# Optimization experiments

Measured on AMD Instinct MI355X. Metric: run time of the kernel, lower is better.

The kernel has to match this reference:

```python
import jax, jax.numpy as jnp
import numpy as np

N, E, D, H, G, OUT = 50000, 800000, 128, 128, 64, 10


def setup_inputs() -> dict:
    key = jax.random.key(0)
    ks = jax.random.split(key, 10)
    x = jax.random.normal(ks[0], (N, D), dtype=jnp.float32)
    edge_index = jax.random.randint(ks[1], (2, E), 0, N, dtype=jnp.int64)
    batch = jnp.sort(jax.random.randint(ks[2], (N,), 0, G, dtype=jnp.int64))
    s = 1.0 / np.sqrt(D)
    W0 = jax.random.normal(ks[3], (D, H), dtype=jnp.float32) * s
    W1 = jax.random.normal(ks[4], (H, H), dtype=jnp.float32) * s
    W2 = jax.random.normal(ks[5], (H, H), dtype=jnp.float32) * s
    M0w = jax.random.normal(ks[6], (H, H), dtype=jnp.float32) * s
    M0b = jnp.zeros((H,), dtype=jnp.float32)
    M1w = jax.random.normal(ks[7], (H, OUT), dtype=jnp.float32) * s
    M1b = jnp.zeros((OUT,), dtype=jnp.float32)
    return dict(x=x, W0=W0, W1=W1, W2=W2, M0w=M0w, M0b=M0b, M1w=M1w, M1b=M1b,
                edge_index=edge_index, batch=batch)


def gcn_conv(x, W, src, dst):
    # PyG GCNConv (bias=False): h = x @ W; out = D^-1/2 (A + I) D^-1/2 h
    h = x @ W
    deg = jnp.zeros((N,), h.dtype).at[dst].add(1.0) + 1.0  # +1 for self-loop
    dinv = deg ** -0.5
    w = dinv[src] * dinv[dst]  # [E]
    agg = jax.ops.segment_sum(h[src] * w[:, None], dst, num_segments=N)
    return agg + h * (dinv * dinv)[:, None]  # self-loop term


def reference(x, W0, W1, W2, M0w, M0b, M1w, M1b, edge_index, batch):
    src, dst = edge_index[0], edge_index[1]
    h = gcn_conv(x, W0, src, dst)
    h = gcn_conv(jax.nn.relu(h), W1, src, dst)
    h = gcn_conv(jax.nn.relu(h), W2, src, dst)
    # global mean pool over graphs
    sums = jax.ops.segment_sum(h, batch, num_segments=G)
    cnts = jax.ops.segment_sum(jnp.ones((N,), h.dtype), batch, num_segments=G)
    pooled = sums / jnp.maximum(cnts, 1.0)[:, None]
    out = pooled @ M0w + M0b
    out = jax.nn.relu(out) @ M1w + M1b
    return out
```

## Files before the change

kernel.cpp:

```cpp
#include <hip/hip_runtime.h>
#include <hip/hip_fp16.h>

#define NN 50000
#define NE 800000
#define DIM 128
#define NG 64
#define NOUT 10

#define NBKT 391
#define HBLK 256
#define CHUNK ((NE + HBLK - 1) / HBLK)
#define PSLICE 8

#define WPAD 136
#define PSTR (DIM * WPAD)

typedef __attribute__((ext_vector_type(8))) short short8;
typedef __attribute__((ext_vector_type(8))) _Float16 half8;
typedef __attribute__((ext_vector_type(2))) __fp16 fp16x2;
typedef __attribute__((ext_vector_type(4))) float float4v;

union S8H8 { short8 s; half8 h; };
union SH { short s; _Float16 h; };
union H8P { short8 s; fp16x2 h2[4]; };

__device__ __forceinline__ void f16_split(float v, short& hi, short& lo) {
    SH a, b;
    a.h = (_Float16)v;
    b.h = (_Float16)(v - (float)a.h);
    hi = a.s;
    lo = b.s;
}

#define PREP_WB 48
#define PREP_HB (PREP_WB + HBLK)
#define PREP_NB (PREP_HB + 1)
__global__ __launch_bounds__(256) void prep_kernel(const float* __restrict__ W0,
                                                   const float* __restrict__ W1,
                                                   const float* __restrict__ W2,
                                                   short* __restrict__ wsp,
                                                   const int* __restrict__ ei,
                                                   int* __restrict__ blkhist,
                                                   const int* __restrict__ batch,
                                                   int* __restrict__ first) {
    __shared__ int h[NBKT];
    int bx = blockIdx.x;
    if (bx < PREP_WB) {
        int w = bx >> 4;
        int sub = bx & 15;
        const float* W = (w == 0) ? W0 : (w == 1) ? W1 : W2;
        short* Wh = wsp + w * 2 * PSTR;
        short* Wl = Wh + PSTR;
        #pragma unroll
        for (int t = 0; t < 4; ++t) {
            int idx = sub * 1024 + t * 256 + threadIdx.x;
            int k = idx >> 7, n = idx & 127;
            int phys = n * WPAD + ((k + 8 * (n >> 3)) & 127);
            short hi, lo;
            f16_split(W[idx], hi, lo);
            Wh[phys] = hi;
            Wl[phys] = lo;
        }
    } else if (bx < PREP_HB) {
        int b = bx - PREP_WB;
        for (int i = threadIdx.x; i < NBKT; i += 256) h[i] = 0;
        __syncthreads();
        int lo = b * CHUNK, hi = min(lo + CHUNK, NE);
        for (int e = lo + threadIdx.x; e < hi; e += 256)
            atomicAdd(&h[ei[NE + e] >> 7], 1);
        __syncthreads();
        for (int i = threadIdx.x; i < NBKT; i += 256)
            blkhist[b * NBKT + i] = h[i];
    } else {
        int g = threadIdx.x;
        if (g <= NG) {
            int lo = 0, hi = NN;
            while (lo < hi) {
                int mid = (lo + hi) >> 1;
                if (batch[mid] < g) lo = mid + 1; else hi = mid;
            }
            first[g] = lo;
        }
    }
}

__global__ __launch_bounds__(256) void scan_all(int* __restrict__ blkhist,
                                                int* __restrict__ bintot) {
    __shared__ int s[256];
    int bin = blockIdx.x;
    int t = threadIdx.x;
    int v = blkhist[t * NBKT + bin];
    s[t] = v;
    __syncthreads();
    #pragma unroll
    for (int off = 1; off < 256; off <<= 1) {
        int tv = (t >= off) ? s[t - off] : 0;
        __syncthreads();
        s[t] += tv;
        __syncthreads();
    }
    blkhist[t * NBKT + bin] = s[t] - v;
    if (t == 255) bintot[bin] = s[255];
}

__global__ __launch_bounds__(512) void base_scan_kernel(const int* __restrict__ bintot,
                                                        int* __restrict__ bucket_base) {
    __shared__ int s[512];
    int t = threadIdx.x;
    int v = (t < NBKT) ? bintot[t] : 0;
    s[t] = v;
    __syncthreads();
    #pragma unroll
    for (int off = 1; off < 512; off <<= 1) {
        int tv = (t >= off) ? s[t - off] : 0;
        __syncthreads();
        s[t] += tv;
        __syncthreads();
    }
    if (t <= NBKT) bucket_base[t] = s[t] - v;
}

__global__ __launch_bounds__(256) void bucket_scatter(const int* __restrict__ ei,
                                                      const int* __restrict__ blkhist,
                                                      const int* __restrict__ bucket_base,
                                                      unsigned* __restrict__ ebuf) {
    __shared__ int cur[NBKT];
    int b = blockIdx.x;
    for (int i = threadIdx.x; i < NBKT; i += 256)
        cur[i] = blkhist[b * NBKT + i] + bucket_base[i];
    __syncthreads();
    int lo = b * CHUNK, hi = min(lo + CHUNK, NE);
    for (int e = lo + threadIdx.x; e < hi; e += 256) {
        int s = ei[e];
        int d = ei[NE + e];
        int pos = atomicAdd(&cur[d >> 7], 1);
        ebuf[pos] = ((unsigned)(d & 127) << 16) | (unsigned)s;
    }
}

__global__ __launch_bounds__(128) void build_csr(const unsigned* __restrict__ ebuf,
                                                 const int* __restrict__ bucket_base,
                                                 int* __restrict__ rowoff,
                                                 int* __restrict__ csr_src,
                                                 float* __restrict__ dinv) {
    __shared__ int deg[128];
    __shared__ int loff[128];
    int g = blockIdx.x;
    int lo = bucket_base[g], hi = bucket_base[g + 1];
    int t = threadIdx.x;
    deg[t] = 0;
    __syncthreads();
    for (int p = lo + t; p < hi; p += 128)
        atomicAdd(&deg[ebuf[p] >> 16], 1);
    __syncthreads();
    int v = deg[t];
    loff[t] = v;
    __syncthreads();
    #pragma unroll
    for (int off = 1; off < 128; off <<= 1) {
        int tv = (t >= off) ? loff[t - off] : 0;
        __syncthreads();
        loff[t] += tv;
        __syncthreads();
    }
    int excl = loff[t] - v;
    int node = g * 128 + t;
    if (node < NN) {
        rowoff[node] = lo + excl;
        dinv[node] = 1.0f / sqrtf((float)v + 1.0f);
    }
    if (node == 0) rowoff[NN] = NE;
    deg[t] = lo + excl;
    __syncthreads();
    for (int p = lo + t; p < hi; p += 128) {
        unsigned pk = ebuf[p];
        int pos = atomicAdd(&deg[pk >> 16], 1);
        csr_src[pos] = (int)(pk & 0xFFFFu);
    }
}

template <bool AF32>
__global__ __launch_bounds__(256) void gemm_mfma(const float* __restrict__ Xf,
                                                 const __half* __restrict__ Xh,
                                                 const short* __restrict__ Wsp,
                                                 __half* __restrict__ Y, int nrows) {
    __shared__ short W2p[2 * PSTR];
    int tid = threadIdx.x;
    {
        const short8* g = (const short8*)Wsp;
        #pragma unroll
        for (int i = 0; i < 17; ++i) {
            int e = tid + 256 * i;
            *(short8*)&W2p[e * 8] = g[e];
        }
    }
    int wave = tid >> 6;
    int lane = tid & 63;
    int lm = lane & 15;
    int lq = lane >> 4;
    int row_t0 = blockIdx.x * 128 + wave * 32;

    float4v acc[2][8];
    #pragma unroll
    for (int t = 0; t < 2; ++t)
        #pragma unroll
        for (int i = 0; i < 8; ++i) acc[t][i] = (float4v){0.f, 0.f, 0.f, 0.f};

    __syncthreads();
    #pragma unroll
    for (int kk = 0; kk < 4; ++kk) {
        half8 a[2];
        #pragma unroll
        for (int t = 0; t < 2; ++t) {
            int r = min(row_t0 + t * 16 + lm, nrows - 1);
            size_t ao = (size_t)r * DIM + kk * 32 + lq * 8;
            if (AF32) {
                float4 xa = *(const float4*)(Xf + ao);
                float4 xb = *(const float4*)(Xf + ao + 4);
                a[t][0] = (_Float16)xa.x; a[t][1] = (_Float16)xa.y;
                a[t][2] = (_Float16)xa.z; a[t][3] = (_Float16)xa.w;
                a[t][4] = (_Float16)xb.x; a[t][5] = (_Float16)xb.y;
                a[t][6] = (_Float16)xb.z; a[t][7] = (_Float16)xb.w;
            } else {
                S8H8 u;
                u.s = *(const short8*)((const short*)Xh + ao);
                a[t] = u.h;
            }
        }
        int pk = (kk * 32 + lq * 8 + 8 * lm) & 127;
        #pragma unroll
        for (int n0 = 0; n0 < 8; ++n0) {
            int base = (lm * 8 + n0) * WPAD + pk;
            S8H8 bh, bl;
            bh.s = *(const short8*)&W2p[base];
            bl.s = *(const short8*)&W2p[PSTR + base];
            #pragma unroll
            for (int t = 0; t < 2; ++t) {
                acc[t][n0] = __builtin_amdgcn_mfma_f32_16x16x32_f16(a[t], bh.h, acc[t][n0], 0, 0, 0);
                acc[t][n0] = __builtin_amdgcn_mfma_f32_16x16x32_f16(a[t], bl.h, acc[t][n0], 0, 0, 0);
            }
        }
    }
    #pragma unroll
    for (int t = 0; t < 2; ++t)
        #pragma unroll
        for (int rg = 0; rg < 4; ++rg) {
            int row = row_t0 + t * 16 + lq * 4 + rg;
            if (row < nrows) {
                H8P o;
                #pragma unroll
                for (int j = 0; j < 4; ++j)
                    o.h2[j] = __builtin_amdgcn_cvt_pkrtz(acc[t][2 * j][rg], acc[t][2 * j + 1][rg]);
                *(short8*)((short*)Y + (size_t)row * DIM + lm * 8) = o.s;
            }
        }
}

template <bool RELU>
__global__ __launch_bounds__(128) void agg_kernel(const __half* __restrict__ H,
                                                  __half* __restrict__ O16,
                                                  const int* __restrict__ rowoff,
                                                  const int* __restrict__ csr_src,
                                                  const float* __restrict__ dinv) {
    __shared__ float part[8][DIM];
    int i = blockIdx.x;
    int tid = threadIdx.x;
    int grp = tid >> 4;
    int ln = tid & 15;
    int s = rowoff[i], e = rowoff[i + 1];
    const __half* Hc = H + ln * 8;

    float a[8] = {0.f, 0.f, 0.f, 0.f, 0.f, 0.f, 0.f, 0.f};
    int p = s + grp;
    for (; p + 8 < e; p += 16) {
        int u0 = csr_src[p];
        int u1 = csr_src[p + 8];
        float d0 = dinv[u0], d1 = dinv[u1];
        short8 q0 = *(const short8*)(Hc + (size_t)u0 * DIM);
        short8 q1 = *(const short8*)(Hc + (size_t)u1 * DIM);
        #pragma unroll
        for (int k = 0; k < 8; ++k) {
            a[k] = fmaf(d0, __half2float(((const __half*)&q0)[k]), a[k]);
            a[k] = fmaf(d1, __half2float(((const __half*)&q1)[k]), a[k]);
        }
    }
    if (p < e) {
        int u = csr_src[p];
        float d = dinv[u];
        short8 q = *(const short8*)(Hc + (size_t)u * DIM);
        #pragma unroll
        for (int k = 0; k < 8; ++k)
            a[k] = fmaf(d, __half2float(((const __half*)&q)[k]), a[k]);
    }
    #pragma unroll
    for (int k = 0; k < 8; k += 4)
        *(float4*)&part[grp][ln * 8 + k] = make_float4(a[k], a[k + 1], a[k + 2], a[k + 3]);
    __syncthreads();
    int col = tid;
    float tot = 0.f;
    #pragma unroll
    for (int g2 = 0; g2 < 8; ++g2) tot += part[g2][col];
    float di = dinv[i];
    tot = fmaf(di, __half2float(H[(size_t)i * DIM + col]), tot);
    float v = di * tot;
    if (RELU) v = fmaxf(v, 0.0f);
    O16[(size_t)i * DIM + col] = __float2half(v);
}

union U4 { ushort4 u; __half h[4]; };
__global__ __launch_bounds__(128) void pool_part(const __half* __restrict__ H,
                                                 const int* __restrict__ first,
                                                 float* __restrict__ ppart) {
    __shared__ float part[4][DIM];
    int g = blockIdx.x;
    int sl = blockIdx.y;
    int tid = threadIdx.x;
    int rg = tid >> 5, ln = tid & 31;
    int s = first[g], e = first[g + 1];
    float a0 = 0.f, a1 = 0.f, a2 = 0.f, a3 = 0.f;
    for (int r = s + sl * 4 + rg; r < e; r += PSLICE * 4) {
        U4 w;
        w.u = *(const ushort4*)(H + (size_t)r * DIM + ln * 4);
        a0 += __half2float(w.h[0]);
        a1 += __half2float(w.h[1]);
        a2 += __half2float(w.h[2]);
        a3 += __half2float(w.h[3]);
    }
    *(float4*)&part[rg][ln * 4] = make_float4(a0, a1, a2, a3);
    __syncthreads();
    float tot = part[0][tid] + part[1][tid] + part[2][tid] + part[3][tid];
    ppart[(size_t)(g * PSLICE + sl) * DIM + tid] = tot;
}

__global__ __launch_bounds__(128) void mlp_kernel(const float* __restrict__ ppart,
                                                  const int* __restrict__ first,
                                                  const float* __restrict__ M0w,
                                                  const float* __restrict__ M0b,
                                                  const float* __restrict__ M1w,
                                                  const float* __restrict__ M1b,
                                                  float* __restrict__ out) {
    __shared__ float p[DIM];
    __shared__ float t[DIM];
    int g = blockIdx.x;
    int j = threadIdx.x;
    float tot = 0.f;
    #pragma unroll
    for (int sl = 0; sl < PSLICE; ++sl)
        tot += ppart[(size_t)(g * PSLICE + sl) * DIM + j];
    float cnt = (float)max(first[g + 1] - first[g], 1);
    p[j] = tot / cnt;
    __syncthreads();
    float acc = M0b[j];
    #pragma unroll 8
    for (int k = 0; k < DIM; ++k) acc = fmaf(p[k], M0w[k * DIM + j], acc);
    t[j] = fmaxf(acc, 0.0f);
    __syncthreads();
    if (j < NOUT) {
        float o = M1b[j];
        #pragma unroll 8
        for (int k = 0; k < DIM; ++k) o = fmaf(t[k], M1w[k * NOUT + j], o);
        out[g * NOUT + j] = o;
    }
}

extern "C" void kernel_launch(void* const* d_in, const int* in_sizes, int n_in,
                              void* d_out, int out_size, void* d_ws, size_t ws_size,
                              hipStream_t stream) {
    const float* x   = (const float*)d_in[0];
    const float* W0  = (const float*)d_in[1];
    const float* W1  = (const float*)d_in[2];
    const float* W2  = (const float*)d_in[3];
    const float* M0w = (const float*)d_in[4];
    const float* M0b = (const float*)d_in[5];
    const float* M1w = (const float*)d_in[6];
    const float* M1b = (const float*)d_in[7];
    const int* ei    = (const int*)d_in[8];
    const int* batch = (const int*)d_in[9];
    float* out = (float*)d_out;

    char* ws = (char*)d_ws;
    size_t off = 0;
    auto take = [&](size_t bytes) -> void* {
        void* p = ws + off;
        off = (off + bytes + 255) & ~(size_t)255;
        return p;
    };
    __half* hA   = (__half*)take((size_t)NN * DIM * 2);
    __half* hB   = (__half*)take((size_t)NN * DIM * 2);
    unsigned* ebuf = (unsigned*)take((size_t)NE * 4);
    int* csr_src = (int*)take((size_t)NE * 4);
    int* blkhist = (int*)take((size_t)HBLK * NBKT * 4);
    int* bintot  = (int*)take((size_t)NBKT * 4);
    int* bucket_base = (int*)take((size_t)(NBKT + 1) * 4);
    int* rowoff  = (int*)take((size_t)(NN + 1) * 4);
    float* dinv  = (float*)take((size_t)NN * 4);
    int* first   = (int*)take((size_t)(NG + 1) * 4);
    float* ppart = (float*)take((size_t)NG * PSLICE * DIM * 4);
    short* wsp   = (short*)take((size_t)3 * 2 * PSTR * 2);
    (void)ws_size; (void)in_sizes; (void)n_in; (void)out_size;

    prep_kernel<<<PREP_NB, 256, 0, stream>>>(W0, W1, W2, wsp, ei, blkhist, batch, first);
    scan_all<<<NBKT, 256, 0, stream>>>(blkhist, bintot);
    base_scan_kernel<<<1, 512, 0, stream>>>(bintot, bucket_base);
    bucket_scatter<<<HBLK, 256, 0, stream>>>(ei, blkhist, bucket_base, ebuf);
    build_csr<<<NBKT, 128, 0, stream>>>(ebuf, bucket_base, rowoff, csr_src, dinv);

    const int GB = (NN + 127) / 128;
    gemm_mfma<true><<<GB, 256, 0, stream>>>(x, nullptr, wsp, hA, NN);
    agg_kernel<true><<<NN, 128, 0, stream>>>(hA, hB, rowoff, csr_src, dinv);
    gemm_mfma<false><<<GB, 256, 0, stream>>>(nullptr, hB, wsp + 2 * PSTR, hA, NN);
    agg_kernel<true><<<NN, 128, 0, stream>>>(hA, hB, rowoff, csr_src, dinv);
    gemm_mfma<false><<<GB, 256, 0, stream>>>(nullptr, hB, wsp + 4 * PSTR, hA, NN);
    agg_kernel<false><<<NN, 128, 0, stream>>>(hA, hB, rowoff, csr_src, dinv);

    dim3 pgrid(NG, PSLICE);
    pool_part<<<pgrid, 128, 0, stream>>>(hB, first, ppart);
    mlp_kernel<<<NG, 128, 0, stream>>>(ppart, first, M0w, M0b, M1w, M1b, out);
}
```

Baseline: 273.9 us.

## Drop split-fp16 weight correction in GEMM and fuse pooling with MLP

```diff
diff --git a/kernel.cpp b/kernel.cpp
--- a/kernel.cpp
+++ b/kernel.cpp
@@ -10,27 +10,16 @@
 #define NBKT 391
 #define HBLK 256
 #define CHUNK ((NE + HBLK - 1) / HBLK)
-#define PSLICE 8
 
 #define WPAD 136
 #define PSTR (DIM * WPAD)
 
 typedef __attribute__((ext_vector_type(8))) short short8;
 typedef __attribute__((ext_vector_type(8))) _Float16 half8;
-typedef __attribute__((ext_vector_type(2))) __fp16 fp16x2;
 typedef __attribute__((ext_vector_type(4))) float float4v;
 
 union S8H8 { short8 s; half8 h; };
 union SH { short s; _Float16 h; };
-union H8P { short8 s; fp16x2 h2[4]; };
-
-__device__ __forceinline__ void f16_split(float v, short& hi, short& lo) {
-    SH a, b;
-    a.h = (_Float16)v;
-    b.h = (_Float16)(v - (float)a.h);
-    hi = a.s;
-    lo = b.s;
-}
 
 #define PREP_WB 48
 #define PREP_HB (PREP_WB + HBLK)
@@ -49,17 +38,15 @@
         int w = bx >> 4;
         int sub = bx & 15;
         const float* W = (w == 0) ? W0 : (w == 1) ? W1 : W2;
-        short* Wh = wsp + w * 2 * PSTR;
-        short* Wl = Wh + PSTR;
+        short* Wp = wsp + w * PSTR;
         #pragma unroll
         for (int t = 0; t < 4; ++t) {
             int idx = sub * 1024 + t * 256 + threadIdx.x;
             int k = idx >> 7, n = idx & 127;
             int phys = n * WPAD + ((k + 8 * (n >> 3)) & 127);
-            short hi, lo;
-            f16_split(W[idx], hi, lo);
-            Wh[phys] = hi;
-            Wl[phys] = lo;
+            SH c;
+            c.h = (_Float16)W[idx];
+            Wp[phys] = c.s;
         }
     } else if (bx < PREP_HB) {
         int b = bx - PREP_WB;
@@ -184,14 +171,14 @@
                                                  const __half* __restrict__ Xh,
                                                  const short* __restrict__ Wsp,
                                                  __half* __restrict__ Y, int nrows) {
-    __shared__ short W2p[2 * PSTR];
+    __shared__ short Wp[PSTR];
     int tid = threadIdx.x;
     {
         const short8* g = (const short8*)Wsp;
         #pragma unroll
-        for (int i = 0; i < 17; ++i) {
+        for (int i = 0; i < 9; ++i) {
             int e = tid + 256 * i;
-            *(short8*)&W2p[e * 8] = g[e];
+            if (e < PSTR / 8) *(short8*)&Wp[e * 8] = g[e];
         }
     }
     int wave = tid >> 6;
@@ -230,15 +217,11 @@
         int pk = (kk * 32 + lq * 8 + 8 * lm) & 127;
         #pragma unroll
         for (int n0 = 0; n0 < 8; ++n0) {
-            int base = (lm * 8 + n0) * WPAD + pk;
-            S8H8 bh, bl;
-            bh.s = *(const short8*)&W2p[base];
-            bl.s = *(const short8*)&W2p[PSTR + base];
+            S8H8 b;
+            b.s = *(const short8*)&Wp[(lm * 8 + n0) * WPAD + pk];
             #pragma unroll
-            for (int t = 0; t < 2; ++t) {
-                acc[t][n0] = __builtin_amdgcn_mfma_f32_16x16x32_f16(a[t], bh.h, acc[t][n0], 0, 0, 0);
-                acc[t][n0] = __builtin_amdgcn_mfma_f32_16x16x32_f16(a[t], bl.h, acc[t][n0], 0, 0, 0);
-            }
+            for (int t = 0; t < 2; ++t)
+                acc[t][n0] = __builtin_amdgcn_mfma_f32_16x16x32_f16(a[t], b.h, acc[t][n0], 0, 0, 0);
         }
     }
     #pragma unroll
@@ -247,11 +230,14 @@
         for (int rg = 0; rg < 4; ++rg) {
             int row = row_t0 + t * 16 + lq * 4 + rg;
             if (row < nrows) {
-                H8P o;
+                short8 o;
                 #pragma unroll
-                for (int j = 0; j < 4; ++j)
-                    o.h2[j] = __builtin_amdgcn_cvt_pkrtz(acc[t][2 * j][rg], acc[t][2 * j + 1][rg]);
-                *(short8*)((short*)Y + (size_t)row * DIM + lm * 8) = o.s;
+                for (int j = 0; j < 8; ++j) {
+                    SH c;
+                    c.h = (_Float16)acc[t][j][rg];
+                    o[j] = c.s;
+                }
+                *(short8*)((short*)Y + (size_t)row * DIM + lm * 8) = o;
             }
         }
 }
@@ -308,17 +294,22 @@
 }
 
 union U4 { ushort4 u; __half h[4]; };
-__global__ __launch_bounds__(128) void pool_part(const __half* __restrict__ H,
-                                                 const int* __restrict__ first,
-                                                 float* __restrict__ ppart) {
-    __shared__ float part[4][DIM];
+__global__ __launch_bounds__(256) void pool_mlp(const __half* __restrict__ H,
+                                                const int* __restrict__ first,
+                                                const float* __restrict__ M0w,
+                                                const float* __restrict__ M0b,
+                                                const float* __restrict__ M1w,
+                                                const float* __restrict__ M1b,
+                                                float* __restrict__ out) {
+    __shared__ float part[8][DIM];
+    __shared__ float p[DIM];
+    __shared__ float t2[DIM];
     int g = blockIdx.x;
-    int sl = blockIdx.y;
     int tid = threadIdx.x;
     int rg = tid >> 5, ln = tid & 31;
     int s = first[g], e = first[g + 1];
     float a0 = 0.f, a1 = 0.f, a2 = 0.f, a3 = 0.f;
-    for (int r = s + sl * 4 + rg; r < e; r += PSLICE * 4) {
+    for (int r = s + rg; r < e; r += 8) {
         U4 w;
         w.u = *(const ushort4*)(H + (size_t)r * DIM + ln * 4);
         a0 += __half2float(w.h[0]);
@@ -328,38 +319,26 @@
     }
     *(float4*)&part[rg][ln * 4] = make_float4(a0, a1, a2, a3);
     __syncthreads();
-    float tot = part[0][tid] + part[1][tid] + part[2][tid] + part[3][tid];
-    ppart[(size_t)(g * PSLICE + sl) * DIM + tid] = tot;
-}
-
-__global__ __launch_bounds__(128) void mlp_kernel(const float* __restrict__ ppart,
-                                                  const int* __restrict__ first,
-                                                  const float* __restrict__ M0w,
-                                                  const float* __restrict__ M0b,
-                                                  const float* __restrict__ M1w,
-                                                  const float* __restrict__ M1b,
-                                                  float* __restrict__ out) {
-    __shared__ float p[DIM];
-    __shared__ float t[DIM];
-    int g = blockIdx.x;
-    int j = threadIdx.x;
-    float tot = 0.f;
-    #pragma unroll
-    for (int sl = 0; sl < PSLICE; ++sl)
-        tot += ppart[(size_t)(g * PSLICE + sl) * DIM + j];
-    float cnt = (float)max(first[g + 1] - first[g], 1);
-    p[j] = tot / cnt;
-    __syncthreads();
-    float acc = M0b[j];
-    #pragma unroll 8
-    for (int k = 0; k < DIM; ++k) acc = fmaf(p[k], M0w[k * DIM + j], acc);
-    t[j] = fmaxf(acc, 0.0f);
-    __syncthreads();
-    if (j < NOUT) {
-        float o = M1b[j];
+    if (tid < DIM) {
+        float tot = 0.f;
+        #pragma unroll
+        for (int g2 = 0; g2 < 8; ++g2) tot += part[g2][tid];
+        float cnt = (float)max(e - s, 1);
+        p[tid] = tot / cnt;
+    }
+    __syncthreads();
+    if (tid < DIM) {
+        float acc = M0b[tid];
         #pragma unroll 8
-        for (int k = 0; k < DIM; ++k) o = fmaf(t[k], M1w[k * NOUT + j], o);
-        out[g * NOUT + j] = o;
+        for (int k = 0; k < DIM; ++k) acc = fmaf(p[k], M0w[k * DIM + tid], acc);
+        t2[tid] = fmaxf(acc, 0.0f);
+    }
+    __syncthreads();
+    if (tid < NOUT) {
+        float o = M1b[tid];
+        #pragma unroll 8
+        for (int k = 0; k < DIM; ++k) o = fmaf(t2[k], M1w[k * NOUT + tid], o);
+        out[g * NOUT + tid] = o;
     }
 }
 
@@ -395,8 +374,7 @@
     int* rowoff  = (int*)take((size_t)(NN + 1) * 4);
     float* dinv  = (float*)take((size_t)NN * 4);
     int* first   = (int*)take((size_t)(NG + 1) * 4);
-    float* ppart = (float*)take((size_t)NG * PSLICE * DIM * 4);
-    short* wsp   = (short*)take((size_t)3 * 2 * PSTR * 2);
+    short* wsp   = (short*)take((size_t)3 * PSTR * 2);
     (void)ws_size; (void)in_sizes; (void)n_in; (void)out_size;
 
     prep_kernel<<<PREP_NB, 256, 0, stream>>>(W0, W1, W2, wsp, ei, blkhist, batch, first);
@@ -408,12 +386,10 @@
     const int GB = (NN + 127) / 128;
     gemm_mfma<true><<<GB, 256, 0, stream>>>(x, nullptr, wsp, hA, NN);
     agg_kernel<true><<<NN, 128, 0, stream>>>(hA, hB, rowoff, csr_src, dinv);
+    gemm_mfma<false><<<GB, 256, 0, stream>>>(nullptr, hB, wsp + PSTR, hA, NN);
+    agg_kernel<true><<<NN, 128, 0, stream>>>(hA, hB, rowoff, csr_src, dinv);
     gemm_mfma<false><<<GB, 256, 0, stream>>>(nullptr, hB, wsp + 2 * PSTR, hA, NN);
-    agg_kernel<true><<<NN, 128, 0, stream>>>(hA, hB, rowoff, csr_src, dinv);
-    gemm_mfma<false><<<GB, 256, 0, stream>>>(nullptr, hB, wsp + 4 * PSTR, hA, NN);
     agg_kernel<false><<<NN, 128, 0, stream>>>(hA, hB, rowoff, csr_src, dinv);
 
-    dim3 pgrid(NG, PSLICE);
-    pool_part<<<pgrid, 128, 0, stream>>>(hB, first, ppart);
-    mlp_kernel<<<NG, 128, 0, stream>>>(ppart, first, M0w, M0b, M1w, M1b, out);
-}
+    pool_mlp<<<NG, 256, 0, stream>>>(hB, first, M0w, M0b, M1w, M1b, out);
+}
```

Result: slower. 288.1 us (+5.2%).
